# Performance work log

Hardware: AMD Instinct MI355X
Metric: run time of the kernel (lower is better)

The kernel has to match this reference:

```python
import jax, jax.numpy as jnp
import numpy as np

B, L, E = 2, 2048, 1024
H = 16
DH = E // H  # head dim for qk and v (dim_qk=dim_v=embed_dim)
HID = 4 * E  # fcn_dim_factor * dim_v
SCALE = DH ** 0.5


def setup_inputs() -> dict:
    key = jax.random.key(0)
    ks = jax.random.split(key, 12)
    s = lambda fan_in: 1.0 / np.sqrt(fan_in)
    return {
        "x": jax.random.uniform(ks[0], (B, L), jnp.float32),
        "z": jax.random.normal(ks[1], (B, L, E), jnp.float32),
        "Wq": jax.random.normal(ks[2], (E, E), jnp.float32) * s(E),
        "bq": jnp.zeros((E,), jnp.float32),
        "Wk": jax.random.normal(ks[3], (E, E), jnp.float32) * s(E),
        "bk": jnp.zeros((E,), jnp.float32),
        "Wv": jax.random.normal(ks[4], (E, E), jnp.float32) * s(E),
        "bv": jnp.zeros((E,), jnp.float32),
        "W1": jax.random.normal(ks[5], (E, HID), jnp.float32) * s(E),
        "b1": jnp.zeros((HID,), jnp.float32),
        "W2": jax.random.normal(ks[6], (HID, 1), jnp.float32) * s(HID),
        "b2": jnp.zeros((1,), jnp.float32),
    }


def reference(x, z, Wq, bq, Wk, bk, Wv, bv, W1, b1, W2, b2):
    # Projections -> (B, H, L, DH)
    def heads(t):
        return t.reshape(B, L, H, DH).transpose(0, 2, 1, 3)

    Q = heads(z @ Wq + bq)
    K = heads(z @ Wk + bk)
    V = heads(z @ Wv + bv)

    # Scores (B, H, L, L)
    S = jnp.einsum("bhid,bhjd->bhij", Q, K) / SCALE

    # Weighted softmax along query axis (dim=-2), weighted by population x
    w = x[:, None, :, None]  # (B, 1, L, 1), broadcasts over queries i
    m = jnp.max(S, axis=-2, keepdims=True)
    e = w * jnp.exp(S - m)
    A = e / jnp.sum(e, axis=-2, keepdims=True)

    # V scaled by population weight, then AV
    V_scaled = w * V
    O = jnp.einsum("bhij,bhjd->bhid", A, V_scaled)  # (B, H, L, DH)
    O = O.transpose(0, 2, 1, 3).reshape(B, L, H * DH)

    # FFN: Linear -> GELU (exact) -> Linear(->1) -> squeeze
    y = jax.nn.gelu(O @ W1 + b1, approximate=False)
    y = (y @ W2 + b2).squeeze(-1)  # (B, L)
    return y
```

## Files before the change

### kernel.cpp

```cpp
#include <hip/hip_runtime.h>
#include <hip/hip_bf16.h>
#include <math.h>

#define B_    2
#define L_    2048
#define E_    1024
#define H_    16
#define DH_   64
#define HID_  4096
#define NROW_ (B_*L_)
#define BH_   (B_*H_)

#define QSCL  0.18033688011112042f

typedef __attribute__((ext_vector_type(8)))  short    short8v;
typedef _Float16 half8v __attribute__((ext_vector_type(8)));
typedef __attribute__((ext_vector_type(16))) float    f32x16;

#define MFMA32(A, Bv, C) __builtin_amdgcn_mfma_f32_32x32x16_bf16((A), (Bv), (C), 0, 0, 0)
#define MFMAH(A, Bv, C)  __builtin_amdgcn_mfma_f32_32x32x16_f16((A), (Bv), (C), 0, 0, 0)

#define WAITV(N) asm volatile("s_waitcnt vmcnt(" #N ")" ::: "memory")
#define SBAR()   __builtin_amdgcn_s_barrier()

__device__ __forceinline__ unsigned short f2bf(float f) {
    union { float f; unsigned u; } v; v.f = f;
    return (unsigned short)((v.u + 0x8000u) >> 16);
}
__device__ __forceinline__ unsigned pack2_bf16(float lo, float hi) {
    union { float f; unsigned u; } a, b; a.f = lo; b.f = hi;
    return __builtin_amdgcn_perm(b.u + 0x8000u, a.u + 0x8000u, 0x07060302u);
}
__device__ __forceinline__ float bf2f(unsigned short u) {
    union { unsigned u; float f; } v; v.u = ((unsigned)u) << 16;
    return v.f;
}

__device__ __forceinline__ void gl_lds16(const void* g, void* l) {
    __builtin_amdgcn_global_load_lds(
        (const __attribute__((address_space(1))) unsigned int*)g,
        (__attribute__((address_space(3))) unsigned int*)l, 16, 0, 0);
}

__device__ __forceinline__ float erf_fast(float v) {
    float a = fabsf(v);
    float t = __builtin_amdgcn_rcpf(1.0f + 0.3275911f * a);
    float p = t * (0.254829592f + t * (-0.284496736f + t * (1.421413741f +
              t * (-1.453152027f + t * 1.061405429f))));
    float r = 1.0f - p * __expf(-a * a);
    return copysignf(r, v);
}

__global__ __launch_bounds__(256) void zh_prep(
    const float* __restrict__ z, _Float16* __restrict__ zh)
{
    const size_t i = ((size_t)blockIdx.x * 256 + threadIdx.x) * 8;
    float4 a = *(const float4*)&z[i];
    float4 b = *(const float4*)&z[i + 4];
    union { _Float16 h[8]; half8v v; } o;
    o.h[0] = (_Float16)a.x; o.h[1] = (_Float16)a.y;
    o.h[2] = (_Float16)a.z; o.h[3] = (_Float16)a.w;
    o.h[4] = (_Float16)b.x; o.h[5] = (_Float16)b.y;
    o.h[6] = (_Float16)b.z; o.h[7] = (_Float16)b.w;
    *(half8v*)&zh[i] = o.v;
}

__global__ __launch_bounds__(256) void wprep3(
    const float* __restrict__ Wq, const float* __restrict__ Wk,
    const float* __restrict__ Wv,
    _Float16* __restrict__ Tq, _Float16* __restrict__ Tk,
    _Float16* __restrict__ Tv)
{
    const float* src = (blockIdx.z == 0) ? Wq : (blockIdx.z == 1) ? Wk : Wv;
    _Float16*    dst = (blockIdx.z == 0) ? Tq : (blockIdx.z == 1) ? Tk : Tv;
    __shared__ float tile[64][65];
    const int t  = threadIdx.x;
    const int r0 = blockIdx.y * 64, c0 = blockIdx.x * 64;
    #pragma unroll
    for (int u = 0; u < 4; ++u) {
        int f = t + 256 * u, row = f >> 4, c4 = (f & 15) << 2;
        *(float4*)&tile[row][c4] = *(const float4*)&src[(size_t)(r0 + row) * E_ + c0 + c4];
    }
    __syncthreads();
    #pragma unroll
    for (int u = 0; u < 4; ++u) {
        int f = t + 256 * u, c = f >> 4, r4 = (f & 15) << 2;
        union { _Float16 h[4]; uint2 u2; } pk;
        pk.h[0] = (_Float16)tile[r4 + 0][c];
        pk.h[1] = (_Float16)tile[r4 + 1][c];
        pk.h[2] = (_Float16)tile[r4 + 2][c];
        pk.h[3] = (_Float16)tile[r4 + 3][c];
        *(uint2*)&dst[(size_t)(c0 + c) * E_ + r0 + r4] = pk.u2;
    }
}

__global__ __launch_bounds__(256) void w1prep(
    const float* __restrict__ W1, _Float16* __restrict__ W1t)
{
    __shared__ float tile[64][65];
    const int t  = threadIdx.x;
    const int r0 = blockIdx.y * 64, c0 = blockIdx.x * 64;
    #pragma unroll
    for (int u = 0; u < 4; ++u) {
        int f = t + 256 * u, row = f >> 4, c4 = (f & 15) << 2;
        *(float4*)&tile[row][c4] = *(const float4*)&W1[(size_t)(r0 + row) * HID_ + c0 + c4];
    }
    __syncthreads();
    #pragma unroll
    for (int u = 0; u < 4; ++u) {
        int f = t + 256 * u, c = f >> 4, r4 = (f & 15) << 2;
        union { _Float16 h[4]; uint2 u2; } pk;
        pk.h[0] = (_Float16)tile[r4 + 0][c];
        pk.h[1] = (_Float16)tile[r4 + 1][c];
        pk.h[2] = (_Float16)tile[r4 + 2][c];
        pk.h[3] = (_Float16)tile[r4 + 3][c];
        *(uint2*)&W1t[(size_t)(c0 + c) * E_ + r0 + r4] = pk.u2;
    }
}

__global__ __launch_bounds__(256) void qkv_mfma(
    const _Float16* __restrict__ zh,
    const _Float16* __restrict__ Tall,
    const float* __restrict__ bq, const float* __restrict__ bk,
    const float* __restrict__ bv,
    unsigned short* __restrict__ outQKV)
{
    const int which = blockIdx.y >> 3;
    const float* bias = (which == 0) ? bq : (which == 1) ? bk : bv;
    const float  osc  = (which == 0) ? QSCL : 1.0f;
    unsigned short* out = outQKV + (size_t)which * ((size_t)BH_ * L_ * DH_);

    __shared__ _Float16 Ah[2][128 * 64];
    __shared__ _Float16 Bs[2][128 * 64];

    const int t    = threadIdx.x;
    const int lane = t & 63;
    const int w    = t >> 6;
    const int l31  = lane & 31;
    const int hq   = lane >> 5;
    const int wm   = w >> 1, wn = w & 1;
    const int m0   = blockIdx.x * 128;
    const int n0   = blockIdx.y * 128;

    const int srow0 = (lane >> 3);
    const int ssl   = lane & 7;

    f32x16 acc[2][2] = {};

#define QKV_STAGE(bb, kc)                                                          \
    {                                                                              \
        _Pragma("unroll")                                                          \
        for (int u = 0; u < 4; ++u) {                                              \
            int ch  = w * 4 + u;                                                   \
            int row = ch * 8 + srow0;                                              \
            gl_lds16(&zh[(size_t)(m0 + row) * E_ + (kc) * 64 + ((ssl ^ (row & 7)) << 3)], \
                     &Ah[bb][ch * 512]);                                           \
            gl_lds16(&Tall[(size_t)(n0 + row) * E_ + (kc) * 64 + ((ssl ^ (row & 7)) << 3)], \
                     &Bs[bb][ch * 512]);                                           \
        }                                                                          \
    }

    QKV_STAGE(0, 0);
    QKV_STAGE(1, 1);
    __syncthreads();
    int cur = 0;

    for (int kc = 0; kc < 16; ++kc) {
        if (kc < 15) WAITV(8); else WAITV(0);
        SBAR();
        __builtin_amdgcn_s_setprio(1);
        #pragma unroll
        for (int ks = 0; ks < 4; ++ks) {
            half8v fb[2];
            #pragma unroll
            for (int nb = 0; nb < 2; ++nb) {
                int br = wn * 64 + nb * 32 + l31;
                fb[nb] = *(const half8v*)&Bs[cur][br * 64 + (((ks * 2 + hq) ^ (br & 7)) << 3)];
            }
            #pragma unroll
            for (int mb = 0; mb < 2; ++mb) {
                int ar = wm * 64 + mb * 32 + l31;
                half8v fa = *(const half8v*)&Ah[cur][ar * 64 + (((ks * 2 + hq) ^ (ar & 7)) << 3)];
                acc[mb][0] = MFMAH(fa, fb[0], acc[mb][0]);
                acc[mb][1] = MFMAH(fa, fb[1], acc[mb][1]);
            }
        }
        __builtin_amdgcn_s_setprio(0);
        SBAR();
        if (kc + 2 < 16) QKV_STAGE(cur, kc + 2);
        cur ^= 1;
    }

    #pragma unroll
    for (int nb = 0; nb < 2; ++nb) {
        int n  = n0 + wn * 64 + nb * 32 + l31;
        int nn = n & 1023;
        int h  = nn >> 6, dh = nn & 63;
        float bb = bias[nn];
        #pragma unroll
        for (int mb = 0; mb < 2; ++mb) {
            #pragma unroll
            for (int r = 0; r < 16; ++r) {
                int m  = m0 + wm * 64 + mb * 32 + (r & 3) + 8 * (r >> 2) + 4 * hq;
                int b  = m >> 11, i = m & (L_ - 1);
                out[((size_t)(b * H_ + h) * L_ + i) * DH_ + dh] = f2bf((acc[mb][nb][r] + bb) * osc);
            }
        }
    }
#undef QKV_STAGE
}

__global__ __launch_bounds__(256) void col_stats_mfma(
    const unsigned short* __restrict__ Qb, const unsigned short* __restrict__ Kb,
    const float* __restrict__ x, float* __restrict__ Do)
{
    __shared__ unsigned short Qlds[2][128 * 64];
    __shared__ float xlds[L_];

    const int t    = threadIdx.x;
    const int lane = t & 63;
    const int wv   = t >> 6;
    const int l31  = lane & 31;
    const int hq   = lane >> 5;
    const int bh   = blockIdx.y;
    const int b    = bh >> 4;
    const int j0   = blockIdx.x * 256 + wv * 64;

    const int srow0 = (lane >> 3);
    const int ssl   = lane & 7;

    #pragma unroll
    for (int u = 0; u < 2; ++u) {
        int f = t + 256 * u;
        *(float4*)&xlds[f * 4] = *(const float4*)&x[(size_t)b * L_ + f * 4];
    }

    short8v kf[2][4];
    #pragma unroll
    for (int s = 0; s < 2; ++s) {
        const unsigned short* kp = Kb + ((size_t)bh * L_ + j0 + s * 32 + l31) * DH_ + hq * 8;
        #pragma unroll
        for (int c = 0; c < 4; ++c) kf[s][c] = *(const short8v*)(kp + c * 16);
    }

    float d0[16], d1[16];
    #pragma unroll
    for (int r = 0; r < 16; ++r) { d0[r] = 0.f; d1[r] = 0.f; }

#define CS_STAGE(bb, ich)                                                           \
    {                                                                               \
        _Pragma("unroll")                                                           \
        for (int u = 0; u < 4; ++u) {                                               \
            int ch  = wv * 4 + u;                                                   \
            int row = ch * 8 + srow0;                                               \
            gl_lds16(&Qb[((size_t)bh * L_ + (ich) * 128 + row) * DH_ + ((ssl ^ (row & 7)) << 3)], \
                     &Qlds[bb][ch * 512]);                                          \
        }                                                                           \
    }

    CS_STAGE(0, 0);
    CS_STAGE(1, 1);
    __syncthreads();
    int cur = 0;

    const int NT = L_ / 128;
    for (int ich = 0; ich < NT; ++ich) {
        if (ich < NT - 1) WAITV(4); else WAITV(0);
        SBAR();
        #pragma unroll
        for (int cc = 0; cc < 4; ++cc) {
            f32x16 a0 = {}, a1 = {};
            __builtin_amdgcn_s_setprio(1);
            #pragma unroll
            for (int c = 0; c < 4; ++c) {
                int qr = cc * 32 + l31;
                short8v qv = *(const short8v*)&Qlds[cur][qr * 64 + (((c * 2 + hq) ^ (qr & 7)) << 3)];
                a0 = MFMA32(kf[0][c], qv, a0);
                a1 = MFMA32(kf[1][c], qv, a1);
            }
            __builtin_amdgcn_s_setprio(0);
            float xi = xlds[ich * 128 + cc * 32 + l31];
            #pragma unroll
            for (int r = 0; r < 16; ++r) {
                d0[r] += xi * __builtin_amdgcn_exp2f(a0[r]);
                d1[r] += xi * __builtin_amdgcn_exp2f(a1[r]);
            }
        }
        SBAR();
        if (ich + 2 < NT) CS_STAGE(cur, ich + 2);
        cur ^= 1;
    }

    #pragma unroll
    for (int r = 0; r < 16; ++r) {
        #pragma unroll
        for (int off = 16; off > 0; off >>= 1) {
            d0[r] += __shfl_xor(d0[r], off);
            d1[r] += __shfl_xor(d1[r], off);
        }
    }
    if (l31 == 0) {
        #pragma unroll
        for (int r = 0; r < 16; ++r) {
            int jr = 4 * hq + (r & 3) + 8 * (r >> 2);
            Do[(size_t)bh * L_ + j0 + jr]      = d0[r];
            Do[(size_t)bh * L_ + j0 + 32 + jr] = d1[r];
        }
    }
#undef CS_STAGE
}

__global__ __launch_bounds__(256) void vt_prep(
    const unsigned short* __restrict__ Vb, const float* __restrict__ x,
    const float* __restrict__ Do, unsigned short* __restrict__ Vt)
{
    const int bh = blockIdx.y;
    const int b  = bh >> 4;
    const int j  = blockIdx.x * 256 + threadIdx.x;
    const float s = x[(size_t)b * L_ + j] / Do[(size_t)bh * L_ + j];
    const unsigned short* vp = Vb + ((size_t)bh * L_ + j) * DH_;
    #pragma unroll
    for (int c = 0; c < 16; ++c) {
        ushort4 v = *(const ushort4*)&vp[c * 4];
        Vt[((size_t)bh * DH_ + c * 4 + 0) * L_ + j] = f2bf(bf2f(v.x) * s);
        Vt[((size_t)bh * DH_ + c * 4 + 1) * L_ + j] = f2bf(bf2f(v.y) * s);
        Vt[((size_t)bh * DH_ + c * 4 + 2) * L_ + j] = f2bf(bf2f(v.z) * s);
        Vt[((size_t)bh * DH_ + c * 4 + 3) * L_ + j] = f2bf(bf2f(v.w) * s);
    }
}

__global__ __launch_bounds__(256) void attn_out_mfma(
    const unsigned short* __restrict__ Qb, const unsigned short* __restrict__ Kb,
    const unsigned short* __restrict__ Vt, const float* __restrict__ x,
    _Float16* __restrict__ Of)
{
    __shared__ unsigned short Klds[2][64 * 64];
    __shared__ unsigned short Vlds[2][64 * 64];

    const int t    = threadIdx.x;
    const int lane = t & 63;
    const int wv   = t >> 6;
    const int l31  = lane & 31;
    const int hq   = lane >> 5;
    const int bh   = blockIdx.y;
    const int b    = bh >> 4, hh = bh & 15;
    const int iw   = blockIdx.x * 128 + wv * 32;

    const int srow0 = (lane >> 3);
    const int ssl   = lane & 7;

    short8v qf[4];
    {
        const unsigned short* qp = Qb + ((size_t)bh * L_ + iw + l31) * DH_ + hq * 8;
        #pragma unroll
        for (int c = 0; c < 4; ++c) qf[c] = *(const short8v*)(qp + c * 16);
    }

    f32x16 accO0 = {}, accO1 = {};

#define AO_STAGE(bb, jt)                                                            \
    {                                                                               \
        _Pragma("unroll")                                                           \
        for (int u = 0; u < 2; ++u) {                                               \
            int ch  = wv * 2 + u;                                                   \
            int row = ch * 8 + srow0;                                               \
            gl_lds16(&Kb[((size_t)bh * L_ + (jt) * 64 + row) * DH_ + ((ssl ^ (row & 7)) << 3)], \
                     &Klds[bb][ch * 512]);                                          \
            gl_lds16(&Vt[((size_t)bh * DH_ + row) * L_ + (jt) * 64 + ((ssl ^ (row & 7)) << 3)], \
                     &Vlds[bb][ch * 512]);                                          \
        }                                                                           \
    }

    AO_STAGE(0, 0);
    AO_STAGE(1, 1);
    __syncthreads();
    int cur = 0;

    const int NT = L_ / 64;
    for (int jt = 0; jt < NT; ++jt) {
        if (jt < NT - 1) WAITV(4); else WAITV(0);
        SBAR();

        uint4 pa[4];
        #pragma unroll
        for (int js = 0; js < 2; ++js) {
            f32x16 as = {};
            __builtin_amdgcn_s_setprio(1);
            #pragma unroll
            for (int c = 0; c < 4; ++c) {
                int krow = js * 32 + l31;
                short8v kfr = *(const short8v*)&Klds[cur][krow * 64 + (((c * 2 + hq) ^ (krow & 7)) << 3)];
                as = MFMA32(kfr, qf[c], as);
            }
            __builtin_amdgcn_s_setprio(0);
            float p[16];
            #pragma unroll
            for (int r = 0; r < 16; ++r) p[r] = __builtin_amdgcn_exp2f(as[r]);

            unsigned P0 = pack2_bf16(p[0], p[1]);
            unsigned P1 = pack2_bf16(p[2], p[3]);
            unsigned Q0 = pack2_bf16(p[4], p[5]);
            unsigned Q1 = pack2_bf16(p[6], p[7]);
            asm("v_permlane32_swap_b32 %0, %1" : "+v"(P0), "+v"(Q0));
            asm("v_permlane32_swap_b32 %0, %1" : "+v"(P1), "+v"(Q1));
            pa[js * 2 + 0] = make_uint4(P0, P1, Q0, Q1);

            unsigned R0 = pack2_bf16(p[8],  p[9]);
            unsigned R1 = pack2_bf16(p[10], p[11]);
            unsigned S0 = pack2_bf16(p[12], p[13]);
            unsigned S1 = pack2_bf16(p[14], p[15]);
            asm("v_permlane32_swap_b32 %0, %1" : "+v"(R0), "+v"(S0));
            asm("v_permlane32_swap_b32 %0, %1" : "+v"(R1), "+v"(S1));
            pa[js * 2 + 1] = make_uint4(R0, R1, S0, S1);
        }

        __builtin_amdgcn_s_setprio(1);
        #pragma unroll
        for (int c = 0; c < 4; ++c) {
            union { uint4 u; short8v s; } paf; paf.u = pa[c];
            int r0 = l31, r1 = 32 + l31;
            short8v vf0 = *(const short8v*)&Vlds[cur][r0 * 64 + (((c * 2 + hq) ^ (r0 & 7)) << 3)];
            short8v vf1 = *(const short8v*)&Vlds[cur][r1 * 64 + (((c * 2 + hq) ^ (r1 & 7)) << 3)];
            accO0 = MFMA32(paf.s, vf0, accO0);
            accO1 = MFMA32(paf.s, vf1, accO1);
        }
        __builtin_amdgcn_s_setprio(0);
        SBAR();
        if (jt + 2 < NT) AO_STAGE(cur, jt + 2);
        cur ^= 1;
    }

    #pragma unroll
    for (int q = 0; q < 4; ++q) {
        float4 xq = *(const float4*)&x[(size_t)b * L_ + iw + 4 * hq + 8 * q];
        const float xs[4] = { xq.x, xq.y, xq.z, xq.w };
        #pragma unroll
        for (int k = 0; k < 4; ++k) {
            int r    = q * 4 + k;
            int irow = iw + 4 * hq + 8 * q + k;
            size_t base = ((size_t)b * L_ + irow) * E_ + hh * DH_;
            Of[base + l31]      = (_Float16)(accO0[r] * xs[k]);
            Of[base + 32 + l31] = (_Float16)(accO1[r] * xs[k]);
        }
    }
#undef AO_STAGE
}

__global__ __launch_bounds__(256) void y_init(float* __restrict__ y, const float* __restrict__ b2)
{
    y[blockIdx.x * 256 + threadIdx.x] = b2[0];
}

__global__ __launch_bounds__(512) void mlp_mfma(
    const _Float16* __restrict__ Of, const _Float16* __restrict__ W1t,
    const float* __restrict__ b1, const float* __restrict__ W2,
    float* __restrict__ y)
{
    __shared__ _Float16 Oh[2][256 * 64];
    __shared__ _Float16 Wh[2][256 * 64];

    const int t    = threadIdx.x;
    const int lane = t & 63;
    const int w    = t >> 6;
    const int l31  = lane & 31;
    const int hq   = lane >> 5;
    const int wm   = w >> 2, wn = w & 3;
    const int m0   = blockIdx.x * 256;
    const int n0   = blockIdx.y * 256;

    const int srow0 = (lane >> 3);
    const int ssl   = lane & 7;

    f32x16 acc[4][2] = {};

#define MLP_STAGE(bb, kc)                                                          \
    {                                                                              \
        _Pragma("unroll")                                                          \
        for (int u = 0; u < 4; ++u) {                                              \
            int ch  = w * 4 + u;                                                   \
            int row = ch * 8 + srow0;                                              \
            gl_lds16(&Of[(size_t)(m0 + row) * E_ + (kc) * 64 + ((ssl ^ (row & 7)) << 3)], \
                     &Oh[bb][ch * 512]);                                           \
            gl_lds16(&W1t[(size_t)(n0 + row) * E_ + (kc) * 64 + ((ssl ^ (row & 7)) << 3)], \
                     &Wh[bb][ch * 512]);                                           \
        }                                                                          \
    }

    MLP_STAGE(0, 0);
    MLP_STAGE(1, 1);
    __syncthreads();
    int cur = 0;

    for (int kc = 0; kc < 16; ++kc) {
        if (kc < 15) WAITV(8); else WAITV(0);
        SBAR();
        __builtin_amdgcn_s_setprio(1);
        #pragma unroll
        for (int ks = 0; ks < 4; ++ks) {
            half8v fb[2];
            #pragma unroll
            for (int nb = 0; nb < 2; ++nb) {
                int br = wn * 64 + nb * 32 + l31;
                fb[nb] = *(const half8v*)&Wh[cur][br * 64 + (((ks * 2 + hq) ^ (br & 7)) << 3)];
            }
            #pragma unroll
            for (int mb = 0; mb < 4; ++mb) {
                int ar = wm * 128 + mb * 32 + l31;
                half8v fa = *(const half8v*)&Oh[cur][ar * 64 + (((ks * 2 + hq) ^ (ar & 7)) << 3)];
                acc[mb][0] = MFMAH(fa, fb[0], acc[mb][0]);
                acc[mb][1] = MFMAH(fa, fb[1], acc[mb][1]);
            }
        }
        __builtin_amdgcn_s_setprio(0);
        SBAR();
        if (kc + 2 < 16) MLP_STAGE(cur, kc + 2);
        cur ^= 1;
    }

    const int hid0 = n0 + wn * 64 + l31;
    const float bb0 = b1[hid0],      w20 = W2[hid0];
    const float bb1 = b1[hid0 + 32], w21 = W2[hid0 + 32];
    #pragma unroll
    for (int mb = 0; mb < 4; ++mb) {
        #pragma unroll
        for (int r = 0; r < 16; ++r) {
            float h0 = acc[mb][0][r] + bb0;
            float h1 = acc[mb][1][r] + bb1;
            float s  = 0.5f * h0 * (1.0f + erf_fast(h0 * 0.70710678f)) * w20
                     + 0.5f * h1 * (1.0f + erf_fast(h1 * 0.70710678f)) * w21;
            #pragma unroll
            for (int off = 16; off > 0; off >>= 1) s += __shfl_xor(s, off);
            if (l31 == 0) {
                int m = m0 + wm * 128 + mb * 32 + (r & 3) + 8 * (r >> 2) + 4 * hq;
                atomicAdd(&y[m], s);
            }
        }
    }
#undef MLP_STAGE
}

extern "C" void kernel_launch(void* const* d_in, const int* in_sizes, int n_in,
                              void* d_out, int out_size, void* d_ws, size_t ws_size,
                              hipStream_t stream)
{
    const float* x  = (const float*)d_in[0];
    const float* z  = (const float*)d_in[1];
    const float* Wq = (const float*)d_in[2];
    const float* bq = (const float*)d_in[3];
    const float* Wk = (const float*)d_in[4];
    const float* bk = (const float*)d_in[5];
    const float* Wv = (const float*)d_in[6];
    const float* bv = (const float*)d_in[7];
    const float* W1 = (const float*)d_in[8];
    const float* b1 = (const float*)d_in[9];
    const float* W2 = (const float*)d_in[10];
    const float* b2 = (const float*)d_in[11];
    float* y = (float*)d_out;

    const size_t NQ = (size_t)BH_ * L_ * DH_;
    unsigned short* p = (unsigned short*)d_ws;
    unsigned short* Qb  = p;  p += NQ;
    unsigned short* Kb  = p;  p += NQ;
    unsigned short* Vb  = p;  p += NQ;
    unsigned short* Vt  = p;  p += NQ;
    _Float16* zh  = (_Float16*)p;  p += (size_t)NROW_ * E_;
    _Float16* Tq  = (_Float16*)p;  p += (size_t)E_ * E_;
    _Float16* Tk  = (_Float16*)p;  p += (size_t)E_ * E_;
    _Float16* Tv  = (_Float16*)p;  p += (size_t)E_ * E_;
    _Float16* W1t = (_Float16*)p;  p += (size_t)HID_ * E_;
    _Float16* Ofp = (_Float16*)p;  p += (size_t)NROW_ * E_;
    float* Dw = (float*)p;

    zh_prep<<<dim3((NROW_ * E_) / (256 * 8)), 256, 0, stream>>>(z, zh);
    wprep3 <<<dim3(E_ / 64, E_ / 64, 3), 256, 0, stream>>>(Wq, Wk, Wv, Tq, Tk, Tv);
    w1prep <<<dim3(HID_ / 64, E_ / 64), 256, 0, stream>>>(W1, W1t);

    qkv_mfma<<<dim3(NROW_ / 128, 3 * E_ / 128), 256, 0, stream>>>(
        zh, Tq, bq, bk, bv, Qb);

    col_stats_mfma<<<dim3(L_ / 256, BH_), 256, 0, stream>>>(Qb, Kb, x, Dw);

    vt_prep<<<dim3(L_ / 256, BH_), 256, 0, stream>>>(Vb, x, Dw, Vt);

    attn_out_mfma<<<dim3(L_ / 128, BH_), 256, 0, stream>>>(Qb, Kb, Vt, x, Ofp);

    y_init<<<dim3(NROW_ / 256), 256, 0, stream>>>(y, b2);

    mlp_mfma<<<dim3(NROW_ / 256, HID_ / 256), 512, 0, stream>>>(
        Ofp, W1t, b1, W2, y);
}
```

Measured before the change: 221.8 us.

## Double query rows per warp in attention and shrink MLP tiles to 128x128

The attention-output kernel now has each warp process two 32-row query groups, so each K/V LDS tile feeds twice as many MFMAs and the grid halves. The MLP GEMM moves from 256x256 tiles with 512 threads to 128x128 tiles with 256 threads, quadrupling block count for better occupancy and load spread. The costs are higher register pressure in attention, and more global re-reads of operands plus more atomics in the MLP.

```diff
diff --git a/kernel.cpp b/kernel.cpp
--- a/kernel.cpp
+++ b/kernel.cpp
@@ -344,19 +344,20 @@
     const int hq   = lane >> 5;
     const int bh   = blockIdx.y;
     const int b    = bh >> 4, hh = bh & 15;
-    const int iw   = blockIdx.x * 128 + wv * 32;
+    const int iw   = blockIdx.x * 256 + wv * 64;
 
     const int srow0 = (lane >> 3);
     const int ssl   = lane & 7;
 
-    short8v qf[4];
-    {
-        const unsigned short* qp = Qb + ((size_t)bh * L_ + iw + l31) * DH_ + hq * 8;
-        #pragma unroll
-        for (int c = 0; c < 4; ++c) qf[c] = *(const short8v*)(qp + c * 16);
-    }
-
-    f32x16 accO0 = {}, accO1 = {};
+    short8v qf[2][4];
+    #pragma unroll
+    for (int ig = 0; ig < 2; ++ig) {
+        const unsigned short* qp = Qb + ((size_t)bh * L_ + iw + ig * 32 + l31) * DH_ + hq * 8;
+        #pragma unroll
+        for (int c = 0; c < 4; ++c) qf[ig][c] = *(const short8v*)(qp + c * 16);
+    }
+
+    f32x16 accO[2][2] = {};
 
 #define AO_STAGE(bb, jt)                                                            \
     {                                                                               \
@@ -381,48 +382,56 @@
         if (jt < NT - 1) WAITV(4); else WAITV(0);
         SBAR();
 
-        uint4 pa[4];
+        uint4 pa[2][4];
         #pragma unroll
         for (int js = 0; js < 2; ++js) {
-            f32x16 as = {};
+            f32x16 as0 = {}, as1 = {};
             __builtin_amdgcn_s_setprio(1);
             #pragma unroll
             for (int c = 0; c < 4; ++c) {
                 int krow = js * 32 + l31;
                 short8v kfr = *(const short8v*)&Klds[cur][krow * 64 + (((c * 2 + hq) ^ (krow & 7)) << 3)];
-                as = MFMA32(kfr, qf[c], as);
+                as0 = MFMA32(kfr, qf[0][c], as0);
+                as1 = MFMA32(kfr, qf[1][c], as1);
             }
             __builtin_amdgcn_s_setprio(0);
-            float p[16];
-            #pragma unroll
-            for (int r = 0; r < 16; ++r) p[r] = __builtin_amdgcn_exp2f(as[r]);
-
-            unsigned P0 = pack2_bf16(p[0], p[1]);
-            unsigned P1 = pack2_bf16(p[2], p[3]);
-            unsigned Q0 = pack2_bf16(p[4], p[5]);
-            unsigned Q1 = pack2_bf16(p[6], p[7]);
-            asm("v_permlane32_swap_b32 %0, %1" : "+v"(P0), "+v"(Q0));
-            asm("v_permlane32_swap_b32 %0, %1" : "+v"(P1), "+v"(Q1));
-            pa[js * 2 + 0] = make_uint4(P0, P1, Q0, Q1);
-
-            unsigned R0 = pack2_bf16(p[8],  p[9]);
-            unsigned R1 = pack2_bf16(p[10], p[11]);
-            unsigned S0 = pack2_bf16(p[12], p[13]);
-            unsigned S1 = pack2_bf16(p[14], p[15]);
-            asm("v_permlane32_swap_b32 %0, %1" : "+v"(R0), "+v"(S0));
-            asm("v_permlane32_swap_b32 %0, %1" : "+v"(R1), "+v"(S1));
-            pa[js * 2 + 1] = make_uint4(R0, R1, S0, S1);
+            #pragma unroll
+            for (int ig = 0; ig < 2; ++ig) {
+                const f32x16& as = (ig == 0) ? as0 : as1;
+                float p[16];
+                #pragma unroll
+                for (int r = 0; r < 16; ++r) p[r] = __builtin_amdgcn_exp2f(as[r]);
+
+                unsigned P0 = pack2_bf16(p[0], p[1]);
+                unsigned P1 = pack2_bf16(p[2], p[3]);
+                unsigned Q0 = pack2_bf16(p[4], p[5]);
+                unsigned Q1 = pack2_bf16(p[6], p[7]);
+                asm("v_permlane32_swap_b32 %0, %1" : "+v"(P0), "+v"(Q0));
+                asm("v_permlane32_swap_b32 %0, %1" : "+v"(P1), "+v"(Q1));
+                pa[ig][js * 2 + 0] = make_uint4(P0, P1, Q0, Q1);
+
+                unsigned R0 = pack2_bf16(p[8],  p[9]);
+                unsigned R1 = pack2_bf16(p[10], p[11]);
+                unsigned S0 = pack2_bf16(p[12], p[13]);
+                unsigned S1 = pack2_bf16(p[14], p[15]);
+                asm("v_permlane32_swap_b32 %0, %1" : "+v"(R0), "+v"(S0));
+                asm("v_permlane32_swap_b32 %0, %1" : "+v"(R1), "+v"(S1));
+                pa[ig][js * 2 + 1] = make_uint4(R0, R1, S0, S1);
+            }
         }
 
         __builtin_amdgcn_s_setprio(1);
         #pragma unroll
         for (int c = 0; c < 4; ++c) {
-            union { uint4 u; short8v s; } paf; paf.u = pa[c];
+            union { uint4 u; short8v s; } pa0, pa1;
+            pa0.u = pa[0][c]; pa1.u = pa[1][c];
             int r0 = l31, r1 = 32 + l31;
             short8v vf0 = *(const short8v*)&Vlds[cur][r0 * 64 + (((c * 2 + hq) ^ (r0 & 7)) << 3)];
             short8v vf1 = *(const short8v*)&Vlds[cur][r1 * 64 + (((c * 2 + hq) ^ (r1 & 7)) << 3)];
-            accO0 = MFMA32(paf.s, vf0, accO0);
-            accO1 = MFMA32(paf.s, vf1, accO1);
+            accO[0][0] = MFMA32(pa0.s, vf0, accO[0][0]);
+            accO[0][1] = MFMA32(pa0.s, vf1, accO[0][1]);
+            accO[1][0] = MFMA32(pa1.s, vf0, accO[1][0]);
+            accO[1][1] = MFMA32(pa1.s, vf1, accO[1][1]);
         }
         __builtin_amdgcn_s_setprio(0);
         SBAR();
@@ -431,16 +440,19 @@
     }
 
     #pragma unroll
-    for (int q = 0; q < 4; ++q) {
-        float4 xq = *(const float4*)&x[(size_t)b * L_ + iw + 4 * hq + 8 * q];
-        const float xs[4] = { xq.x, xq.y, xq.z, xq.w };
-        #pragma unroll
-        for (int k = 0; k < 4; ++k) {
-            int r    = q * 4 + k;
-            int irow = iw + 4 * hq + 8 * q + k;
-            size_t base = ((size_t)b * L_ + irow) * E_ + hh * DH_;
-            Of[base + l31]      = (_Float16)(accO0[r] * xs[k]);
-            Of[base + 32 + l31] = (_Float16)(accO1[r] * xs[k]);
+    for (int ig = 0; ig < 2; ++ig) {
+        #pragma unroll
+        for (int q = 0; q < 4; ++q) {
+            float4 xq = *(const float4*)&x[(size_t)b * L_ + iw + ig * 32 + 4 * hq + 8 * q];
+            const float xs[4] = { xq.x, xq.y, xq.z, xq.w };
+            #pragma unroll
+            for (int k = 0; k < 4; ++k) {
+                int r    = q * 4 + k;
+                int irow = iw + ig * 32 + 4 * hq + 8 * q + k;
+                size_t base = ((size_t)b * L_ + irow) * E_ + hh * DH_;
+                Of[base + l31]      = (_Float16)(accO[ig][0][r] * xs[k]);
+                Of[base + 32 + l31] = (_Float16)(accO[ig][1][r] * xs[k]);
+            }
         }
     }
 #undef AO_STAGE
@@ -451,27 +463,27 @@
     y[blockIdx.x * 256 + threadIdx.x] = b2[0];
 }
 
-__global__ __launch_bounds__(512) void mlp_mfma(
+__global__ __launch_bounds__(256) void mlp_mfma(
     const _Float16* __restrict__ Of, const _Float16* __restrict__ W1t,
     const float* __restrict__ b1, const float* __restrict__ W2,
     float* __restrict__ y)
 {
-    __shared__ _Float16 Oh[2][256 * 64];
-    __shared__ _Float16 Wh[2][256 * 64];
+    __shared__ _Float16 Oh[2][128 * 64];
+    __shared__ _Float16 Wh[2][128 * 64];
 
     const int t    = threadIdx.x;
     const int lane = t & 63;
     const int w    = t >> 6;
     const int l31  = lane & 31;
     const int hq   = lane >> 5;
-    const int wm   = w >> 2, wn = w & 3;
-    const int m0   = blockIdx.x * 256;
-    const int n0   = blockIdx.y * 256;
+    const int wm   = w >> 1, wn = w & 1;
+    const int m0   = blockIdx.x * 128;
+    const int n0   = blockIdx.y * 128;
 
     const int srow0 = (lane >> 3);
     const int ssl   = lane & 7;
 
-    f32x16 acc[4][2] = {};
+    f32x16 acc[2][2] = {};
 
 #define MLP_STAGE(bb, kc)                                                          \
     {                                                                              \
@@ -504,8 +516,8 @@
                 fb[nb] = *(const half8v*)&Wh[cur][br * 64 + (((ks * 2 + hq) ^ (br & 7)) << 3)];
             }
             #pragma unroll
-            for (int mb = 0; mb < 4; ++mb) {
-                int ar = wm * 128 + mb * 32 + l31;
+            for (int mb = 0; mb < 2; ++mb) {
+                int ar = wm * 64 + mb * 32 + l31;
                 half8v fa = *(const half8v*)&Oh[cur][ar * 64 + (((ks * 2 + hq) ^ (ar & 7)) << 3)];
                 acc[mb][0] = MFMAH(fa, fb[0], acc[mb][0]);
                 acc[mb][1] = MFMAH(fa, fb[1], acc[mb][1]);
@@ -521,7 +533,7 @@
     const float bb0 = b1[hid0],      w20 = W2[hid0];
     const float bb1 = b1[hid0 + 32], w21 = W2[hid0 + 32];
     #pragma unroll
-    for (int mb = 0; mb < 4; ++mb) {
+    for (int mb = 0; mb < 2; ++mb) {
         #pragma unroll
         for (int r = 0; r < 16; ++r) {
             float h0 = acc[mb][0][r] + bb0;
@@ -531,7 +543,7 @@
             #pragma unroll
             for (int off = 16; off > 0; off >>= 1) s += __shfl_xor(s, off);
             if (l31 == 0) {
-                int m = m0 + wm * 128 + mb * 32 + (r & 3) + 8 * (r >> 2) + 4 * hq;
+                int m = m0 + wm * 64 + mb * 32 + (r & 3) + 8 * (r >> 2) + 4 * hq;
                 atomicAdd(&y[m], s);
             }
         }
@@ -582,10 +594,10 @@
 
     vt_prep<<<dim3(L_ / 256, BH_), 256, 0, stream>>>(Vb, x, Dw, Vt);
 
-    attn_out_mfma<<<dim3(L_ / 128, BH_), 256, 0, stream>>>(Qb, Kb, Vt, x, Ofp);
+    attn_out_mfma<<<dim3(L_ / 256, BH_), 256, 0, stream>>>(Qb, Kb, Vt, x, Ofp);
 
     y_init<<<dim3(NROW_ / 256), 256, 0, stream>>>(y, b2);
 
-    mlp_mfma<<<dim3(NROW_ / 256, HID_ / 256), 512, 0, stream>>>(
+    mlp_mfma<<<dim3(NROW_ / 128, HID_ / 128), 256, 0, stream>>>(
         Ofp, W1t, b1, W2, y);
 }
```

Result: faster. 217.4 us (-2.0%).
